# Performance work log

Hardware: AMD Instinct MI355X
Metric: run time of the kernel (lower is better)

## Reference

```python
import jax, jax.numpy as jnp
import numpy as np

N_NODES = 100000


def _graph_conv_right(feat, src, dst, W, b, n_nodes):
    # DGL GraphConv(norm='right'): since in_feats > out_feats, apply weight first,
    # then sum-aggregate messages over edges, divide by in-degree (clamped >= 1),
    # add bias, then relu activation.
    h = feat @ W                                   # [N, out]
    msg = jnp.take(h, src, axis=0)                 # [E, out] gather from source nodes
    agg = jax.ops.segment_sum(msg, dst, num_segments=n_nodes)  # [N, out]
    deg = jax.ops.segment_sum(jnp.ones_like(dst, dtype=feat.dtype), dst,
                              num_segments=n_nodes)
    deg = jnp.clip(deg, 1.0, None)                 # allow_zero_in_degree
    out = agg / deg[:, None] + b
    return jax.nn.relu(out)


def setup_inputs() -> dict:
    key = jax.random.key(0)
    ks = jax.random.split(key, 6)
    n_edges = 3200000
    in_dim, hidden_dim, out_dim = 128, 32, 12
    features = jax.random.normal(ks[0], (N_NODES, in_dim), dtype=jnp.float32)
    src = jax.random.randint(ks[1], (n_edges,), 0, N_NODES, dtype=jnp.int64 if jax.config.jax_enable_x64 else jnp.int32)
    dst = jax.random.randint(ks[2], (n_edges,), 0, N_NODES, dtype=jnp.int64 if jax.config.jax_enable_x64 else jnp.int32)
    W1 = jax.random.normal(ks[3], (in_dim, hidden_dim), dtype=jnp.float32) * (1.0 / np.sqrt(in_dim))
    b1 = jnp.zeros((hidden_dim,), dtype=jnp.float32)
    W2 = jax.random.normal(ks[4], (hidden_dim, out_dim), dtype=jnp.float32) * (1.0 / np.sqrt(hidden_dim))
    b2 = jnp.zeros((out_dim,), dtype=jnp.float32)
    return {"features": features, "src": src, "dst": dst,
            "W1": W1, "b1": b1, "W2": W2, "b2": b2}


def reference(features, src, dst, W1, b1, W2, b2):
    x = _graph_conv_right(features, src, dst, W1, b1, N_NODES)
    x = jax.nn.relu(x)  # extra F.relu after layer1 (idempotent, kept for fidelity)
    x = _graph_conv_right(x, src, dst, W2, b2, N_NODES)
    return x
```

## Files before the change

### kernel.cpp

```cpp
#include <hip/hip_runtime.h>
#include <hip/hip_fp16.h>

#define N_IN   128
#define HID    32
#define ODIM   12
#define H2P    16
#define RNODES 128
#define RSH    7
#define NBMAX  800
#define NBK    1024
#define BCAP   4608
#define CHUNK  4096

__device__ __forceinline__ void acc_f4(float (&acc)[8], float4 vf) {
    union { float4 f; __half2 h[4]; } uu; uu.f = vf;
    float2 g0 = __half22float2(uu.h[0]);
    float2 g1 = __half22float2(uu.h[1]);
    float2 g2 = __half22float2(uu.h[2]);
    float2 g3 = __half22float2(uu.h[3]);
    acc[0] += g0.x; acc[1] += g0.y;
    acc[2] += g1.x; acc[3] += g1.y;
    acc[4] += g2.x; acc[5] += g2.y;
    acc[6] += g3.x; acc[7] += g3.y;
}

__global__ __launch_bounds__(256) void gemm1_kernel(const float* __restrict__ feat,
                                                    const float* __restrict__ W1,
                                                    __half* __restrict__ h1,
                                                    int* __restrict__ bcur, int nNodes) {
    if (blockIdx.x == 0) {
        ((int4*)bcur)[threadIdx.x] = make_int4(0, 0, 0, 0);
    }
    __shared__ float sF[64 * 132];
    __shared__ float sW[N_IN * HID];
    const int tid = threadIdx.x;
    const int nb  = blockIdx.x * 64;

    {
        const float4* Wv  = (const float4*)W1;
        float4*       sWv = (float4*)sW;
        #pragma unroll
        for (int i = 0; i < 4; ++i) sWv[tid + 256 * i] = Wv[tid + 256 * i];
    }
    #pragma unroll
    for (int i = 0; i < 8; ++i) {
        int f   = tid + 256 * i;
        int row = f >> 5;
        int c4  = f & 31;
        int n   = nb + row;
        float4 v = make_float4(0.f, 0.f, 0.f, 0.f);
        if (n < nNodes) v = *(const float4*)(feat + (size_t)n * N_IN + c4 * 4);
        *(float4*)(sF + row * 132 + c4 * 4) = v;
    }
    __syncthreads();

    const int og = tid & 7;
    const int ng = tid >> 3;
    const int o0 = og * 4;
    const float* f0 = sF + ng * 132;
    const float* f1 = sF + (ng + 32) * 132;

    float acc0[4] = {0.f, 0.f, 0.f, 0.f};
    float acc1[4] = {0.f, 0.f, 0.f, 0.f};
    #pragma unroll 8
    for (int k = 0; k < N_IN; k += 4) {
        float4 a0 = *(const float4*)(f0 + k);
        float4 a1 = *(const float4*)(f1 + k);
        const float a0v[4] = {a0.x, a0.y, a0.z, a0.w};
        const float a1v[4] = {a1.x, a1.y, a1.z, a1.w};
        #pragma unroll
        for (int j = 0; j < 4; ++j) {
            float4 w = *(const float4*)(sW + (k + j) * HID + o0);
            acc0[0] += a0v[j] * w.x; acc0[1] += a0v[j] * w.y;
            acc0[2] += a0v[j] * w.z; acc0[3] += a0v[j] * w.w;
            acc1[0] += a1v[j] * w.x; acc1[1] += a1v[j] * w.y;
            acc1[2] += a1v[j] * w.z; acc1[3] += a1v[j] * w.w;
        }
    }
    int n0 = nb + ng, n1 = nb + ng + 32;
    if (n0 < nNodes) {
        union { __half2 h[2]; float2 f; } u;
        u.h[0] = __floats2half2_rn(acc0[0], acc0[1]);
        u.h[1] = __floats2half2_rn(acc0[2], acc0[3]);
        *(float2*)(h1 + (size_t)n0 * HID + o0) = u.f;
    }
    if (n1 < nNodes) {
        union { __half2 h[2]; float2 f; } u;
        u.h[0] = __floats2half2_rn(acc1[0], acc1[1]);
        u.h[1] = __floats2half2_rn(acc1[2], acc1[3]);
        *(float2*)(h1 + (size_t)n1 * HID + o0) = u.f;
    }
}

__global__ __launch_bounds__(512) void bplace_kernel(const int* __restrict__ src,
                                                     const int* __restrict__ dst,
                                                     int* __restrict__ bcur,
                                                     int* __restrict__ pairs, int nEdges) {
    __shared__ int      lh[NBK];
    __shared__ int      lcur[NBK];
    __shared__ int      gofs[NBK];
    __shared__ int      sWS[16];
    __shared__ int      lst[CHUNK];
    __shared__ unsigned short lbk[CHUNK];

    const int tid  = threadIdx.x;
    const int base = blockIdx.x * CHUNK;
    const int m    = min(CHUNK, nEdges - base);

    ((int2*)lh)[tid] = make_int2(0, 0);
    __syncthreads();

    int4 dv[2], sv[2];
    bool ok[2];
    #pragma unroll
    for (int k = 0; k < 2; ++k) {
        int e = base + k * 2048 + tid * 4;
        ok[k] = (e < nEdges);
        if (ok[k]) {
            dv[k] = *(const int4*)(dst + e);
            sv[k] = *(const int4*)(src + e);
        }
    }
    #pragma unroll
    for (int k = 0; k < 2; ++k) {
        if (ok[k]) {
            atomicAdd(&lh[dv[k].x >> RSH], 1);
            atomicAdd(&lh[dv[k].y >> RSH], 1);
            atomicAdd(&lh[dv[k].z >> RSH], 1);
            atomicAdd(&lh[dv[k].w >> RSH], 1);
        }
    }
    __syncthreads();

    int c0 = lh[2 * tid], c1 = lh[2 * tid + 1];
    int tsum = c0 + c1;
    const int lane = tid & 63, wid = tid >> 6;
    int inc = tsum;
    #pragma unroll
    for (int off = 1; off < 64; off <<= 1) {
        int t = __shfl_up(inc, off, 64);
        if (lane >= off) inc += t;
    }
    if (lane == 63) sWS[wid] = inc;
    __syncthreads();
    if (tid == 0) {
        int r = 0;
        #pragma unroll
        for (int w = 0; w < 8; ++w) { int s = sWS[w]; sWS[8 + w] = r; r += s; }
    }
    __syncthreads();
    int excl = sWS[8 + wid] + inc - tsum;
    lh[2 * tid]       = excl;
    lh[2 * tid + 1]   = excl + c0;
    lcur[2 * tid]     = excl;
    lcur[2 * tid + 1] = excl + c0;
    gofs[2 * tid]     = (c0 > 0) ? atomicAdd(&bcur[2 * tid], c0) : 0;
    gofs[2 * tid + 1] = (c1 > 0) ? atomicAdd(&bcur[2 * tid + 1], c1) : 0;
    __syncthreads();

    #pragma unroll
    for (int k = 0; k < 2; ++k) {
        if (ok[k]) {
            int b, p;
            b = dv[k].x >> RSH; p = atomicAdd(&lcur[b], 1); lst[p] = ((dv[k].x & (RNODES - 1)) << 17) | sv[k].x; lbk[p] = (unsigned short)b;
            b = dv[k].y >> RSH; p = atomicAdd(&lcur[b], 1); lst[p] = ((dv[k].y & (RNODES - 1)) << 17) | sv[k].y; lbk[p] = (unsigned short)b;
            b = dv[k].z >> RSH; p = atomicAdd(&lcur[b], 1); lst[p] = ((dv[k].z & (RNODES - 1)) << 17) | sv[k].z; lbk[p] = (unsigned short)b;
            b = dv[k].w >> RSH; p = atomicAdd(&lcur[b], 1); lst[p] = ((dv[k].w & (RNODES - 1)) << 17) | sv[k].w; lbk[p] = (unsigned short)b;
        }
    }
    __syncthreads();

    for (int i = tid; i < m; i += 512) {
        int b = lbk[i];
        int rank = gofs[b] + (i - lh[b]);
        if (rank < BCAP) pairs[(size_t)b * BCAP + rank] = lst[i];
    }
}

__global__ __launch_bounds__(512) void agg1_kernel(const __half* __restrict__ h1,
                                                   const int* __restrict__ bcur,
                                                   int* __restrict__ pairs,
                                                   const float* __restrict__ b1,
                                                   const float* __restrict__ W2,
                                                   __half* __restrict__ h2,
                                                   float* __restrict__ rdeg,
                                                   int* __restrict__ rowstartg,
                                                   int* __restrict__ countg, int nNodes) {
    __shared__ int   sorted[BCAP];
    __shared__ int   hist[RNODES];
    __shared__ int   scn[RNODES];
    __shared__ int   cur[RNODES];
    __shared__ int   sws[2];
    __shared__ float sW2[HID * ODIM];
    const int tid = threadIdx.x;
    const int bkt = blockIdx.x;
    const int cnt = min(bcur[bkt], BCAP);
    const size_t pb = (size_t)bkt * BCAP;

    if (tid < RNODES) hist[tid] = 0;
    if (tid < 96) ((float4*)sW2)[tid] = ((const float4*)W2)[tid];
    __syncthreads();

    int vreg[9];
    #pragma unroll
    for (int u = 0; u < 9; ++u) {
        int i = tid + u * 512;
        if (i < cnt) {
            int v = pairs[pb + i];
            vreg[u] = v;
            atomicAdd(&hist[v >> 17], 1);
        }
    }
    __syncthreads();

    int v0 = 0, inc = 0;
    if (tid < RNODES) {
        v0 = hist[tid];
        inc = v0;
        #pragma unroll
        for (int off = 1; off < 64; off <<= 1) {
            int t = __shfl_up(inc, off, 64);
            if ((tid & 63) >= off) inc += t;
        }
        if ((tid & 63) == 63) sws[tid >> 6] = inc;
    }
    __syncthreads();
    if (tid < RNODES) {
        int add = (tid >= 64) ? sws[0] : 0;
        scn[tid] = add + inc - v0;
        cur[tid] = add + inc - v0;
    }
    __syncthreads();

    #pragma unroll
    for (int u = 0; u < 9; ++u) {
        int i = tid + u * 512;
        if (i < cnt) {
            int v = vreg[u];
            int pos = atomicAdd(&cur[v >> 17], 1);
            sorted[pos] = v & 0x1FFFF;
        }
    }
    __syncthreads();

    for (int i = tid; i < cnt; i += 512) pairs[pb + i] = sorted[i];
    if (tid < RNODES) {
        int n = bkt * RNODES + tid;
        if (n < nNodes) {
            rowstartg[n] = (int)pb + scn[tid];
            countg[n]    = hist[tid];
        }
    }

    const int r   = tid & 7;
    const int grp = tid >> 3;
    const int q   = r & 3;
    const int sub = r >> 2;
    const float4* h1q = (const float4*)h1;

    #pragma unroll
    for (int g = 0; g < 2; ++g) {
        const int nl = g * 64 + grp;
        const int n  = bkt * RNODES + nl;
        if (n >= nNodes) continue;
        const int dcnt = hist[nl];
        const int beg  = scn[nl];
        const int end  = beg + dcnt;

        float acc[8] = {0.f, 0.f, 0.f, 0.f, 0.f, 0.f, 0.f, 0.f};
        int i = beg;
        for (; i + 16 <= end; i += 16) {
            float4 v[8];
            #pragma unroll
            for (int u = 0; u < 8; ++u) {
                int e = sorted[i + 2 * u + sub];
                v[u] = h1q[(size_t)e * 4 + q];
            }
            #pragma unroll
            for (int u = 0; u < 8; ++u) acc_f4(acc, v[u]);
        }
        for (; i + 2 <= end; i += 2) {
            int e = sorted[i + sub];
            acc_f4(acc, h1q[(size_t)e * 4 + q]);
        }
        if (i < end && sub == 0) {
            int e = sorted[i];
            acc_f4(acc, h1q[(size_t)e * 4 + q]);
        }

        #pragma unroll
        for (int t = 0; t < 8; ++t) acc[t] += __shfl_xor(acc[t], 4, 8);

        const float rd = 1.f / (float)(dcnt < 1 ? 1 : dcnt);
        float x[8];
        #pragma unroll
        for (int t = 0; t < 8; ++t) {
            float xv = acc[t] * rd + b1[8 * q + t];
            x[t] = xv > 0.f ? xv : 0.f;
        }

        const int j0  = r;
        const int j1m = (r < 4) ? (r + 8) : r;
        float o0 = 0.f, o1 = 0.f;
        #pragma unroll
        for (int qq = 0; qq < 4; ++qq) {
            #pragma unroll
            for (int t = 0; t < 8; ++t) {
                float xv = __shfl(x[t], qq, 8);
                int k = 8 * qq + t;
                o0 += xv * sW2[k * ODIM + j0];
                o1 += xv * sW2[k * ODIM + j1m];
            }
        }
        h2[(size_t)n * H2P + j0] = __float2half(o0);
        if (r < 4) h2[(size_t)n * H2P + 8 + r] = __float2half(o1);
        if (r == 0) rdeg[n] = rd;
    }
}

__global__ __launch_bounds__(512) void agg2_kernel(const __half* __restrict__ h2,
                                                   const int* __restrict__ rowstartg,
                                                   const int* __restrict__ countg,
                                                   const int* __restrict__ eidx,
                                                   const float* __restrict__ rdeg,
                                                   const float* __restrict__ b2,
                                                   float* __restrict__ out, int nNodes) {
    const int tid = threadIdx.x;
    const int grp = tid >> 3;
    const int r   = tid & 7;
    const int n   = blockIdx.x * 64 + grp;
    if (n >= nNodes) return;

    const int half = r & 1;
    const int sub  = r >> 1;
    const float4* h2q = (const float4*)h2;

    const int cnt = countg[n];
    const int beg = rowstartg[n];
    const int end = beg + cnt;

    float acc[8] = {0.f, 0.f, 0.f, 0.f, 0.f, 0.f, 0.f, 0.f};
    int i = beg;
    for (; i + 32 <= end; i += 32) {
        float4 v[8];
        #pragma unroll
        for (int u = 0; u < 8; ++u) {
            int e = eidx[i + 4 * u + sub];
            v[u] = h2q[(size_t)e * 2 + half];
        }
        #pragma unroll
        for (int u = 0; u < 8; ++u) acc_f4(acc, v[u]);
    }
    for (; i + 4 <= end; i += 4) {
        int e = eidx[i + sub];
        acc_f4(acc, h2q[(size_t)e * 2 + half]);
    }
    const int rem = end - i;
    if (sub < rem) {
        int e = eidx[i + sub];
        acc_f4(acc, h2q[(size_t)e * 2 + half]);
    }

    #pragma unroll
    for (int t = 0; t < 8; ++t) {
        acc[t] += __shfl_xor(acc[t], 2, 8);
        acc[t] += __shfl_xor(acc[t], 4, 8);
    }

    const float rd = rdeg[n];
    if (r == 0) {
        float w[8];
        #pragma unroll
        for (int t = 0; t < 8; ++t) {
            float wv = acc[t] * rd + b2[t];
            w[t] = wv > 0.f ? wv : 0.f;
        }
        *(float4*)(out + (size_t)n * ODIM)     = make_float4(w[0], w[1], w[2], w[3]);
        *(float4*)(out + (size_t)n * ODIM + 4) = make_float4(w[4], w[5], w[6], w[7]);
    } else if (r == 1) {
        float w[4];
        #pragma unroll
        for (int t = 0; t < 4; ++t) {
            float wv = acc[t] * rd + b2[8 + t];
            w[t] = wv > 0.f ? wv : 0.f;
        }
        *(float4*)(out + (size_t)n * ODIM + 8) = make_float4(w[0], w[1], w[2], w[3]);
    }
}

extern "C" void kernel_launch(void* const* d_in, const int* in_sizes, int n_in,
                              void* d_out, int out_size, void* d_ws, size_t ws_size,
                              hipStream_t stream) {
    const float* feat = (const float*)d_in[0];
    const int*   src  = (const int*)d_in[1];
    const int*   dst  = (const int*)d_in[2];
    const float* W1   = (const float*)d_in[3];
    const float* b1   = (const float*)d_in[4];
    const float* W2   = (const float*)d_in[5];
    const float* b2   = (const float*)d_in[6];
    float* out = (float*)d_out;

    const int nEdges = in_sizes[1];
    const int nNodes = in_sizes[0] / N_IN;
    const int nb     = (nNodes + RNODES - 1) / RNODES;

    __half* h1       = (__half*)d_ws;
    __half* h2       = h1 + (size_t)nNodes * HID;
    float*  rdeg     = (float*)(h2 + (size_t)nNodes * H2P);
    int*    rowstart = (int*)(rdeg + nNodes);
    int*    countg   = rowstart + nNodes;
    int*    bcur     = countg + nNodes;
    int*    pairs    = bcur + NBK;

    gemm1_kernel<<<(nNodes + 63) / 64, 256, 0, stream>>>(feat, W1, h1, bcur, nNodes);
    bplace_kernel<<<(nEdges + CHUNK - 1) / CHUNK, 512, 0, stream>>>(src, dst, bcur, pairs, nEdges);
    agg1_kernel<<<nb, 512, 0, stream>>>(h1, bcur, pairs, b1, W2, h2, rdeg, rowstart, countg, nNodes);
    agg2_kernel<<<(nNodes + 63) / 64, 512, 0, stream>>>(h2, rowstart, countg, pairs, rdeg, b2, out, nNodes);
}
```

Before: 238.2 us.

## Split agg1 into sort and gather kernels, enlarge bplace chunks, shrink blocks

The fused per-bucket sort-and-aggregate kernel is split into a sort_kernel that writes sorted source indices and row offsets to global memory, and a separate gather1_kernel with 256-thread blocks covering 32 nodes each. This spreads the layer-1 gather over far more blocks than the 782 buckets, so more of the GPU stays busy, at the cost of one extra launch and a global round trip for the sorted indices. bplace now handles 6400 edges per block (three int4 loads plus a scalar tail), which cuts the block count and the global atomics on bucket cursors. The rdeg buffer is dropped and the reciprocal degree is recomputed in agg2, which also moves to 256-thread blocks.

Result: faster. 225.7 us (-5.2%).

```diff
diff --git a/kernel.cpp b/kernel.cpp
--- a/kernel.cpp
+++ b/kernel.cpp
@@ -10,7 +10,7 @@
 #define NBMAX  800
 #define NBK    1024
 #define BCAP   4608
-#define CHUNK  4096
+#define CHUNK  6400
 
 __device__ __forceinline__ void acc_f4(float (&acc)[8], float4 vf) {
     union { float4 f; __half2 h[4]; } uu; uu.f = vf;
@@ -110,10 +110,10 @@
     ((int2*)lh)[tid] = make_int2(0, 0);
     __syncthreads();
 
-    int4 dv[2], sv[2];
-    bool ok[2];
-    #pragma unroll
-    for (int k = 0; k < 2; ++k) {
+    int4 dv[3], sv[3];
+    bool ok[3];
+    #pragma unroll
+    for (int k = 0; k < 3; ++k) {
         int e = base + k * 2048 + tid * 4;
         ok[k] = (e < nEdges);
         if (ok[k]) {
@@ -121,8 +121,14 @@
             sv[k] = *(const int4*)(src + e);
         }
     }
-    #pragma unroll
-    for (int k = 0; k < 2; ++k) {
+    int  dt = 0, st = 0;
+    bool okt = (tid < 256) && (base + 6144 + tid < nEdges);
+    if (okt) {
+        dt = dst[base + 6144 + tid];
+        st = src[base + 6144 + tid];
+    }
+    #pragma unroll
+    for (int k = 0; k < 3; ++k) {
         if (ok[k]) {
             atomicAdd(&lh[dv[k].x >> RSH], 1);
             atomicAdd(&lh[dv[k].y >> RSH], 1);
@@ -130,6 +136,7 @@
             atomicAdd(&lh[dv[k].w >> RSH], 1);
         }
     }
+    if (okt) atomicAdd(&lh[dt >> RSH], 1);
     __syncthreads();
 
     int c0 = lh[2 * tid], c1 = lh[2 * tid + 1];
@@ -159,7 +166,7 @@
     __syncthreads();
 
     #pragma unroll
-    for (int k = 0; k < 2; ++k) {
+    for (int k = 0; k < 3; ++k) {
         if (ok[k]) {
             int b, p;
             b = dv[k].x >> RSH; p = atomicAdd(&lcur[b], 1); lst[p] = ((dv[k].x & (RNODES - 1)) << 17) | sv[k].x; lbk[p] = (unsigned short)b;
@@ -168,6 +175,10 @@
             b = dv[k].w >> RSH; p = atomicAdd(&lcur[b], 1); lst[p] = ((dv[k].w & (RNODES - 1)) << 17) | sv[k].w; lbk[p] = (unsigned short)b;
         }
     }
+    if (okt) {
+        int b = dt >> RSH, p = atomicAdd(&lcur[b], 1);
+        lst[p] = ((dt & (RNODES - 1)) << 17) | st; lbk[p] = (unsigned short)b;
+    }
     __syncthreads();
 
     for (int i = tid; i < m; i += 512) {
@@ -177,28 +188,21 @@
     }
 }
 
-__global__ __launch_bounds__(512) void agg1_kernel(const __half* __restrict__ h1,
-                                                   const int* __restrict__ bcur,
+__global__ __launch_bounds__(512) void sort_kernel(const int* __restrict__ bcur,
                                                    int* __restrict__ pairs,
-                                                   const float* __restrict__ b1,
-                                                   const float* __restrict__ W2,
-                                                   __half* __restrict__ h2,
-                                                   float* __restrict__ rdeg,
                                                    int* __restrict__ rowstartg,
                                                    int* __restrict__ countg, int nNodes) {
-    __shared__ int   sorted[BCAP];
-    __shared__ int   hist[RNODES];
-    __shared__ int   scn[RNODES];
-    __shared__ int   cur[RNODES];
-    __shared__ int   sws[2];
-    __shared__ float sW2[HID * ODIM];
+    __shared__ int sorted[BCAP];
+    __shared__ int hist[RNODES];
+    __shared__ int scn[RNODES];
+    __shared__ int cur[RNODES];
+    __shared__ int sws[2];
     const int tid = threadIdx.x;
     const int bkt = blockIdx.x;
     const int cnt = min(bcur[bkt], BCAP);
     const size_t pb = (size_t)bkt * BCAP;
 
     if (tid < RNODES) hist[tid] = 0;
-    if (tid < 96) ((float4*)sW2)[tid] = ((const float4*)W2)[tid];
     __syncthreads();
 
     int vreg[9];
@@ -251,84 +255,91 @@
             countg[n]    = hist[tid];
         }
     }
+}
+
+__global__ __launch_bounds__(256) void gather1_kernel(const __half* __restrict__ h1,
+                                                      const int* __restrict__ rowstartg,
+                                                      const int* __restrict__ countg,
+                                                      const int* __restrict__ eidx,
+                                                      const float* __restrict__ b1,
+                                                      const float* __restrict__ W2,
+                                                      __half* __restrict__ h2, int nNodes) {
+    __shared__ float sW2[HID * ODIM];
+    const int tid = threadIdx.x;
+    if (tid < 96) ((float4*)sW2)[tid] = ((const float4*)W2)[tid];
+    __syncthreads();
 
     const int r   = tid & 7;
     const int grp = tid >> 3;
     const int q   = r & 3;
     const int sub = r >> 2;
+    const int n   = blockIdx.x * 32 + grp;
+    if (n >= nNodes) return;
+
     const float4* h1q = (const float4*)h1;
-
-    #pragma unroll
-    for (int g = 0; g < 2; ++g) {
-        const int nl = g * 64 + grp;
-        const int n  = bkt * RNODES + nl;
-        if (n >= nNodes) continue;
-        const int dcnt = hist[nl];
-        const int beg  = scn[nl];
-        const int end  = beg + dcnt;
-
-        float acc[8] = {0.f, 0.f, 0.f, 0.f, 0.f, 0.f, 0.f, 0.f};
-        int i = beg;
-        for (; i + 16 <= end; i += 16) {
-            float4 v[8];
-            #pragma unroll
-            for (int u = 0; u < 8; ++u) {
-                int e = sorted[i + 2 * u + sub];
-                v[u] = h1q[(size_t)e * 4 + q];
-            }
-            #pragma unroll
-            for (int u = 0; u < 8; ++u) acc_f4(acc, v[u]);
-        }
-        for (; i + 2 <= end; i += 2) {
-            int e = sorted[i + sub];
-            acc_f4(acc, h1q[(size_t)e * 4 + q]);
-        }
-        if (i < end && sub == 0) {
-            int e = sorted[i];
-            acc_f4(acc, h1q[(size_t)e * 4 + q]);
-        }
-
-        #pragma unroll
-        for (int t = 0; t < 8; ++t) acc[t] += __shfl_xor(acc[t], 4, 8);
-
-        const float rd = 1.f / (float)(dcnt < 1 ? 1 : dcnt);
-        float x[8];
+    const int dcnt = countg[n];
+    const int beg  = rowstartg[n];
+    const int end  = beg + dcnt;
+
+    float acc[8] = {0.f, 0.f, 0.f, 0.f, 0.f, 0.f, 0.f, 0.f};
+    int i = beg;
+    for (; i + 16 <= end; i += 16) {
+        float4 v[8];
+        #pragma unroll
+        for (int u = 0; u < 8; ++u) {
+            int e = eidx[i + 2 * u + sub];
+            v[u] = h1q[(size_t)e * 4 + q];
+        }
+        #pragma unroll
+        for (int u = 0; u < 8; ++u) acc_f4(acc, v[u]);
+    }
+    for (; i + 2 <= end; i += 2) {
+        int e = eidx[i + sub];
+        acc_f4(acc, h1q[(size_t)e * 4 + q]);
+    }
+    if (i < end && sub == 0) {
+        int e = eidx[i];
+        acc_f4(acc, h1q[(size_t)e * 4 + q]);
+    }
+
+    #pragma unroll
+    for (int t = 0; t < 8; ++t) acc[t] += __shfl_xor(acc[t], 4, 8);
+
+    const float rd = 1.f / (float)(dcnt < 1 ? 1 : dcnt);
+    float x[8];
+    #pragma unroll
+    for (int t = 0; t < 8; ++t) {
+        float xv = acc[t] * rd + b1[8 * q + t];
+        x[t] = xv > 0.f ? xv : 0.f;
+    }
+
+    const int j0  = r;
+    const int j1m = (r < 4) ? (r + 8) : r;
+    float o0 = 0.f, o1 = 0.f;
+    #pragma unroll
+    for (int qq = 0; qq < 4; ++qq) {
         #pragma unroll
         for (int t = 0; t < 8; ++t) {
-            float xv = acc[t] * rd + b1[8 * q + t];
-            x[t] = xv > 0.f ? xv : 0.f;
-        }
-
-        const int j0  = r;
-        const int j1m = (r < 4) ? (r + 8) : r;
-        float o0 = 0.f, o1 = 0.f;
-        #pragma unroll
-        for (int qq = 0; qq < 4; ++qq) {
-            #pragma unroll
-            for (int t = 0; t < 8; ++t) {
-                float xv = __shfl(x[t], qq, 8);
-                int k = 8 * qq + t;
-                o0 += xv * sW2[k * ODIM + j0];
-                o1 += xv * sW2[k * ODIM + j1m];
-            }
-        }
-        h2[(size_t)n * H2P + j0] = __float2half(o0);
-        if (r < 4) h2[(size_t)n * H2P + 8 + r] = __float2half(o1);
-        if (r == 0) rdeg[n] = rd;
-    }
-}
-
-__global__ __launch_bounds__(512) void agg2_kernel(const __half* __restrict__ h2,
+            float xv = __shfl(x[t], qq, 8);
+            int k = 8 * qq + t;
+            o0 += xv * sW2[k * ODIM + j0];
+            o1 += xv * sW2[k * ODIM + j1m];
+        }
+    }
+    h2[(size_t)n * H2P + j0] = __float2half(o0);
+    if (r < 4) h2[(size_t)n * H2P + 8 + r] = __float2half(o1);
+}
+
+__global__ __launch_bounds__(256) void agg2_kernel(const __half* __restrict__ h2,
                                                    const int* __restrict__ rowstartg,
                                                    const int* __restrict__ countg,
                                                    const int* __restrict__ eidx,
-                                                   const float* __restrict__ rdeg,
                                                    const float* __restrict__ b2,
                                                    float* __restrict__ out, int nNodes) {
     const int tid = threadIdx.x;
     const int grp = tid >> 3;
     const int r   = tid & 7;
-    const int n   = blockIdx.x * 64 + grp;
+    const int n   = blockIdx.x * 32 + grp;
     if (n >= nNodes) return;
 
     const int half = r & 1;
@@ -367,7 +378,7 @@
         acc[t] += __shfl_xor(acc[t], 4, 8);
     }
 
-    const float rd = rdeg[n];
+    const float rd = 1.f / (float)(cnt < 1 ? 1 : cnt);
     if (r == 0) {
         float w[8];
         #pragma unroll
@@ -406,14 +417,14 @@
 
     __half* h1       = (__half*)d_ws;
     __half* h2       = h1 + (size_t)nNodes * HID;
-    float*  rdeg     = (float*)(h2 + (size_t)nNodes * H2P);
-    int*    rowstart = (int*)(rdeg + nNodes);
+    int*    rowstart = (int*)(h2 + (size_t)nNodes * H2P);
     int*    countg   = rowstart + nNodes;
     int*    bcur     = countg + nNodes;
     int*    pairs    = bcur + NBK;
 
     gemm1_kernel<<<(nNodes + 63) / 64, 256, 0, stream>>>(feat, W1, h1, bcur, nNodes);
     bplace_kernel<<<(nEdges + CHUNK - 1) / CHUNK, 512, 0, stream>>>(src, dst, bcur, pairs, nEdges);
-    agg1_kernel<<<nb, 512, 0, stream>>>(h1, bcur, pairs, b1, W2, h2, rdeg, rowstart, countg, nNodes);
-    agg2_kernel<<<(nNodes + 63) / 64, 512, 0, stream>>>(h2, rowstart, countg, pairs, rdeg, b2, out, nNodes);
-}
+    sort_kernel<<<nb, 512, 0, stream>>>(bcur, pairs, rowstart, countg, nNodes);
+    gather1_kernel<<<(nNodes + 31) / 32, 256, 0, stream>>>(h1, rowstart, countg, pairs, b1, W2, h2, nNodes);
+    agg2_kernel<<<(nNodes + 31) / 32, 256, 0, stream>>>(h2, rowstart, countg, pairs, b2, out, nNodes);
+}
```

## Split buckets into half-blocks and re-sort edges in LDS per layer

Applied to the files above, without the earlier changes.

The two aggregation kernels now run two blocks per 128-node bucket, each covering 64 nodes. Each block rebuilds its own per-node CSR in shared memory from the bucketed pairs. This removes the sorted-pairs writeback and the global rowstart, count and rdeg arrays, and doubles the number of blocks for parallelism. Layer 1 aggregation now gives each node 16 lanes that each read a half2 per edge, and the W2 matmul uses shuffles. The placement chunk is doubled to 8192 edges per block. The cost is sorting twice (once per layer) and a per-half cap of 2560 edges, which could drop edges on skewed graphs.

Result: faster. 225.5 us (-5.3%).

```diff
diff --git a/kernel.cpp b/kernel.cpp
--- a/kernel.cpp
+++ b/kernel.cpp
@@ -10,7 +10,8 @@
 #define NBMAX  800
 #define NBK    1024
 #define BCAP   4608
-#define CHUNK  4096
+#define HCAP   2560
+#define CHUNK  8192
 
 __device__ __forceinline__ void acc_f4(float (&acc)[8], float4 vf) {
     union { float4 f; __half2 h[4]; } uu; uu.f = vf;
@@ -110,10 +111,10 @@
     ((int2*)lh)[tid] = make_int2(0, 0);
     __syncthreads();
 
-    int4 dv[2], sv[2];
-    bool ok[2];
-    #pragma unroll
-    for (int k = 0; k < 2; ++k) {
+    int4 dv[4], sv[4];
+    bool ok[4];
+    #pragma unroll
+    for (int k = 0; k < 4; ++k) {
         int e = base + k * 2048 + tid * 4;
         ok[k] = (e < nEdges);
         if (ok[k]) {
@@ -122,7 +123,7 @@
         }
     }
     #pragma unroll
-    for (int k = 0; k < 2; ++k) {
+    for (int k = 0; k < 4; ++k) {
         if (ok[k]) {
             atomicAdd(&lh[dv[k].x >> RSH], 1);
             atomicAdd(&lh[dv[k].y >> RSH], 1);
@@ -159,7 +160,7 @@
     __syncthreads();
 
     #pragma unroll
-    for (int k = 0; k < 2; ++k) {
+    for (int k = 0; k < 4; ++k) {
         if (ok[k]) {
             int b, p;
             b = dv[k].x >> RSH; p = atomicAdd(&lcur[b], 1); lst[p] = ((dv[k].x & (RNODES - 1)) << 17) | sv[k].x; lbk[p] = (unsigned short)b;
@@ -177,27 +178,24 @@
     }
 }
 
-__global__ __launch_bounds__(512) void agg1_kernel(const __half* __restrict__ h1,
-                                                   const int* __restrict__ bcur,
-                                                   int* __restrict__ pairs,
-                                                   const float* __restrict__ b1,
-                                                   const float* __restrict__ W2,
-                                                   __half* __restrict__ h2,
-                                                   float* __restrict__ rdeg,
-                                                   int* __restrict__ rowstartg,
-                                                   int* __restrict__ countg, int nNodes) {
-    __shared__ int   sorted[BCAP];
-    __shared__ int   hist[RNODES];
-    __shared__ int   scn[RNODES];
-    __shared__ int   cur[RNODES];
-    __shared__ int   sws[2];
+__global__ __launch_bounds__(512) void l1_kernel(const __half* __restrict__ h1,
+                                                 const int* __restrict__ bcur,
+                                                 const int* __restrict__ pairs,
+                                                 const float* __restrict__ b1,
+                                                 const float* __restrict__ W2,
+                                                 __half* __restrict__ h2, int nNodes) {
+    __shared__ int   sorted[HCAP];
+    __shared__ int   hist[64];
+    __shared__ int   scn[64];
+    __shared__ int   cur[64];
     __shared__ float sW2[HID * ODIM];
     const int tid = threadIdx.x;
-    const int bkt = blockIdx.x;
+    const int bkt = blockIdx.x >> 1;
+    const int h   = blockIdx.x & 1;
     const int cnt = min(bcur[bkt], BCAP);
     const size_t pb = (size_t)bkt * BCAP;
 
-    if (tid < RNODES) hist[tid] = 0;
+    if (tid < 64) hist[tid] = 0;
     if (tid < 96) ((float4*)sW2)[tid] = ((const float4*)W2)[tid];
     __syncthreads();
 
@@ -208,27 +206,20 @@
         if (i < cnt) {
             int v = pairs[pb + i];
             vreg[u] = v;
-            atomicAdd(&hist[v >> 17], 1);
-        }
-    }
-    __syncthreads();
-
-    int v0 = 0, inc = 0;
-    if (tid < RNODES) {
-        v0 = hist[tid];
-        inc = v0;
+            if (((v >> 17) >> 6) == h) atomicAdd(&hist[(v >> 17) & 63], 1);
+        }
+    }
+    __syncthreads();
+
+    if (tid < 64) {
+        int v0 = hist[tid], inc = v0;
         #pragma unroll
         for (int off = 1; off < 64; off <<= 1) {
             int t = __shfl_up(inc, off, 64);
-            if ((tid & 63) >= off) inc += t;
-        }
-        if ((tid & 63) == 63) sws[tid >> 6] = inc;
-    }
-    __syncthreads();
-    if (tid < RNODES) {
-        int add = (tid >= 64) ? sws[0] : 0;
-        scn[tid] = add + inc - v0;
-        cur[tid] = add + inc - v0;
+            if (tid >= off) inc += t;
+        }
+        scn[tid] = inc - v0;
+        cur[tid] = inc - v0;
     }
     __syncthreads();
 
@@ -237,107 +228,145 @@
         int i = tid + u * 512;
         if (i < cnt) {
             int v = vreg[u];
-            int pos = atomicAdd(&cur[v >> 17], 1);
-            sorted[pos] = v & 0x1FFFF;
-        }
-    }
-    __syncthreads();
-
-    for (int i = tid; i < cnt; i += 512) pairs[pb + i] = sorted[i];
-    if (tid < RNODES) {
-        int n = bkt * RNODES + tid;
-        if (n < nNodes) {
-            rowstartg[n] = (int)pb + scn[tid];
-            countg[n]    = hist[tid];
-        }
-    }
-
-    const int r   = tid & 7;
-    const int grp = tid >> 3;
-    const int q   = r & 3;
-    const int sub = r >> 2;
-    const float4* h1q = (const float4*)h1;
+            if (((v >> 17) >> 6) == h) {
+                int pos = atomicAdd(&cur[(v >> 17) & 63], 1);
+                if (pos < HCAP) sorted[pos] = v & 0x1FFFF;
+            }
+        }
+    }
+    __syncthreads();
+
+    const int c   = tid & 15;
+    const int grp = tid >> 4;
+    const __half2* h1v = (const __half2*)h1;
+    const int col = (c < ODIM) ? c : 0;
 
     #pragma unroll
     for (int g = 0; g < 2; ++g) {
-        const int nl = g * 64 + grp;
-        const int n  = bkt * RNODES + nl;
+        int nl = g * 32 + grp;
+        int n  = bkt * RNODES + h * 64 + nl;
         if (n >= nNodes) continue;
-        const int dcnt = hist[nl];
-        const int beg  = scn[nl];
-        const int end  = beg + dcnt;
-
-        float acc[8] = {0.f, 0.f, 0.f, 0.f, 0.f, 0.f, 0.f, 0.f};
+        int dcnt = hist[nl];
+        int beg  = scn[nl];
+        int end  = beg + dcnt;
+
+        float2 s0 = {0.f, 0.f}, s1 = {0.f, 0.f}, s2 = {0.f, 0.f}, s3 = {0.f, 0.f};
         int i = beg;
-        for (; i + 16 <= end; i += 16) {
-            float4 v[8];
-            #pragma unroll
-            for (int u = 0; u < 8; ++u) {
-                int e = sorted[i + 2 * u + sub];
-                v[u] = h1q[(size_t)e * 4 + q];
+        for (; i + 8 <= end; i += 8) {
+            int e0 = sorted[i],     e1 = sorted[i + 1], e2 = sorted[i + 2], e3 = sorted[i + 3];
+            int e4 = sorted[i + 4], e5 = sorted[i + 5], e6 = sorted[i + 6], e7 = sorted[i + 7];
+            float2 f0 = __half22float2(h1v[(size_t)e0 * 16 + c]);
+            float2 f1 = __half22float2(h1v[(size_t)e1 * 16 + c]);
+            float2 f2 = __half22float2(h1v[(size_t)e2 * 16 + c]);
+            float2 f3 = __half22float2(h1v[(size_t)e3 * 16 + c]);
+            float2 f4 = __half22float2(h1v[(size_t)e4 * 16 + c]);
+            float2 f5 = __half22float2(h1v[(size_t)e5 * 16 + c]);
+            float2 f6 = __half22float2(h1v[(size_t)e6 * 16 + c]);
+            float2 f7 = __half22float2(h1v[(size_t)e7 * 16 + c]);
+            s0.x += f0.x; s0.y += f0.y;  s1.x += f1.x; s1.y += f1.y;
+            s2.x += f2.x; s2.y += f2.y;  s3.x += f3.x; s3.y += f3.y;
+            s0.x += f4.x; s0.y += f4.y;  s1.x += f5.x; s1.y += f5.y;
+            s2.x += f6.x; s2.y += f6.y;  s3.x += f7.x; s3.y += f7.y;
+        }
+        for (; i + 4 <= end; i += 4) {
+            int e0 = sorted[i], e1 = sorted[i + 1], e2 = sorted[i + 2], e3 = sorted[i + 3];
+            float2 f0 = __half22float2(h1v[(size_t)e0 * 16 + c]);
+            float2 f1 = __half22float2(h1v[(size_t)e1 * 16 + c]);
+            float2 f2 = __half22float2(h1v[(size_t)e2 * 16 + c]);
+            float2 f3 = __half22float2(h1v[(size_t)e3 * 16 + c]);
+            s0.x += f0.x; s0.y += f0.y;  s1.x += f1.x; s1.y += f1.y;
+            s2.x += f2.x; s2.y += f2.y;  s3.x += f3.x; s3.y += f3.y;
+        }
+        for (; i < end; ++i) {
+            float2 f = __half22float2(h1v[(size_t)sorted[i] * 16 + c]);
+            s0.x += f.x; s0.y += f.y;
+        }
+        float sumx = (s0.x + s1.x) + (s2.x + s3.x);
+        float sumy = (s0.y + s1.y) + (s2.y + s3.y);
+
+        float rd = 1.f / (float)(dcnt < 1 ? 1 : dcnt);
+        float x0 = sumx * rd + b1[2 * c];
+        float x1 = sumy * rd + b1[2 * c + 1];
+        x0 = x0 > 0.f ? x0 : 0.f;
+        x1 = x1 > 0.f ? x1 : 0.f;
+
+        float acc = 0.f;
+        #pragma unroll
+        for (int k = 0; k < 16; ++k) {
+            float xk0 = __shfl(x0, k, 16);
+            float xk1 = __shfl(x1, k, 16);
+            acc += xk0 * sW2[(2 * k) * ODIM + col] + xk1 * sW2[(2 * k + 1) * ODIM + col];
+        }
+        if (c < ODIM) h2[(size_t)n * H2P + c] = __float2half(acc);
+    }
+}
+
+__global__ __launch_bounds__(512) void l2_kernel(const __half* __restrict__ h2,
+                                                 const int* __restrict__ bcur,
+                                                 const int* __restrict__ pairs,
+                                                 const float* __restrict__ b2,
+                                                 float* __restrict__ out, int nNodes) {
+    __shared__ int sorted[HCAP];
+    __shared__ int hist[64];
+    __shared__ int scn[64];
+    __shared__ int cur[64];
+    const int tid = threadIdx.x;
+    const int bkt = blockIdx.x >> 1;
+    const int h   = blockIdx.x & 1;
+    const int cnt = min(bcur[bkt], BCAP);
+    const size_t pb = (size_t)bkt * BCAP;
+
+    if (tid < 64) hist[tid] = 0;
+    __syncthreads();
+
+    int vreg[9];
+    #pragma unroll
+    for (int u = 0; u < 9; ++u) {
+        int i = tid + u * 512;
+        if (i < cnt) {
+            int v = pairs[pb + i];
+            vreg[u] = v;
+            if (((v >> 17) >> 6) == h) atomicAdd(&hist[(v >> 17) & 63], 1);
+        }
+    }
+    __syncthreads();
+
+    if (tid < 64) {
+        int v0 = hist[tid], inc = v0;
+        #pragma unroll
+        for (int off = 1; off < 64; off <<= 1) {
+            int t = __shfl_up(inc, off, 64);
+            if (tid >= off) inc += t;
+        }
+        scn[tid] = inc - v0;
+        cur[tid] = inc - v0;
+    }
+    __syncthreads();
+
+    #pragma unroll
+    for (int u = 0; u < 9; ++u) {
+        int i = tid + u * 512;
+        if (i < cnt) {
+            int v = vreg[u];
+            if (((v >> 17) >> 6) == h) {
+                int pos = atomicAdd(&cur[(v >> 17) & 63], 1);
+                if (pos < HCAP) sorted[pos] = v & 0x1FFFF;
             }
-            #pragma unroll
-            for (int u = 0; u < 8; ++u) acc_f4(acc, v[u]);
-        }
-        for (; i + 2 <= end; i += 2) {
-            int e = sorted[i + sub];
-            acc_f4(acc, h1q[(size_t)e * 4 + q]);
-        }
-        if (i < end && sub == 0) {
-            int e = sorted[i];
-            acc_f4(acc, h1q[(size_t)e * 4 + q]);
-        }
-
-        #pragma unroll
-        for (int t = 0; t < 8; ++t) acc[t] += __shfl_xor(acc[t], 4, 8);
-
-        const float rd = 1.f / (float)(dcnt < 1 ? 1 : dcnt);
-        float x[8];
-        #pragma unroll
-        for (int t = 0; t < 8; ++t) {
-            float xv = acc[t] * rd + b1[8 * q + t];
-            x[t] = xv > 0.f ? xv : 0.f;
-        }
-
-        const int j0  = r;
-        const int j1m = (r < 4) ? (r + 8) : r;
-        float o0 = 0.f, o1 = 0.f;
-        #pragma unroll
-        for (int qq = 0; qq < 4; ++qq) {
-            #pragma unroll
-            for (int t = 0; t < 8; ++t) {
-                float xv = __shfl(x[t], qq, 8);
-                int k = 8 * qq + t;
-                o0 += xv * sW2[k * ODIM + j0];
-                o1 += xv * sW2[k * ODIM + j1m];
-            }
-        }
-        h2[(size_t)n * H2P + j0] = __float2half(o0);
-        if (r < 4) h2[(size_t)n * H2P + 8 + r] = __float2half(o1);
-        if (r == 0) rdeg[n] = rd;
-    }
-}
-
-__global__ __launch_bounds__(512) void agg2_kernel(const __half* __restrict__ h2,
-                                                   const int* __restrict__ rowstartg,
-                                                   const int* __restrict__ countg,
-                                                   const int* __restrict__ eidx,
-                                                   const float* __restrict__ rdeg,
-                                                   const float* __restrict__ b2,
-                                                   float* __restrict__ out, int nNodes) {
-    const int tid = threadIdx.x;
-    const int grp = tid >> 3;
-    const int r   = tid & 7;
-    const int n   = blockIdx.x * 64 + grp;
-    if (n >= nNodes) return;
-
+        }
+    }
+    __syncthreads();
+
+    const int r    = tid & 7;
+    const int nl   = tid >> 3;
     const int half = r & 1;
     const int sub  = r >> 1;
+    const int n    = bkt * RNODES + h * 64 + nl;
+    if (n >= nNodes) return;
+
     const float4* h2q = (const float4*)h2;
-
-    const int cnt = countg[n];
-    const int beg = rowstartg[n];
-    const int end = beg + cnt;
+    const int dcnt = hist[nl];
+    const int beg  = scn[nl];
+    const int end  = beg + dcnt;
 
     float acc[8] = {0.f, 0.f, 0.f, 0.f, 0.f, 0.f, 0.f, 0.f};
     int i = beg;
@@ -345,19 +374,19 @@
         float4 v[8];
         #pragma unroll
         for (int u = 0; u < 8; ++u) {
-            int e = eidx[i + 4 * u + sub];
+            int e = sorted[i + 4 * u + sub];
             v[u] = h2q[(size_t)e * 2 + half];
         }
         #pragma unroll
         for (int u = 0; u < 8; ++u) acc_f4(acc, v[u]);
     }
     for (; i + 4 <= end; i += 4) {
-        int e = eidx[i + sub];
+        int e = sorted[i + sub];
         acc_f4(acc, h2q[(size_t)e * 2 + half]);
     }
     const int rem = end - i;
     if (sub < rem) {
-        int e = eidx[i + sub];
+        int e = sorted[i + sub];
         acc_f4(acc, h2q[(size_t)e * 2 + half]);
     }
 
@@ -367,7 +396,7 @@
         acc[t] += __shfl_xor(acc[t], 4, 8);
     }
 
-    const float rd = rdeg[n];
+    const float rd = 1.f / (float)(dcnt < 1 ? 1 : dcnt);
     if (r == 0) {
         float w[8];
         #pragma unroll
@@ -403,17 +432,15 @@
     const int nEdges = in_sizes[1];
     const int nNodes = in_sizes[0] / N_IN;
     const int nb     = (nNodes + RNODES - 1) / RNODES;
-
-    __half* h1       = (__half*)d_ws;
-    __half* h2       = h1 + (size_t)nNodes * HID;
-    float*  rdeg     = (float*)(h2 + (size_t)nNodes * H2P);
-    int*    rowstart = (int*)(rdeg + nNodes);
-    int*    countg   = rowstart + nNodes;
-    int*    bcur     = countg + nNodes;
-    int*    pairs    = bcur + NBK;
+    const int hbGrid = 2 * nb;
+
+    __half* h1    = (__half*)d_ws;
+    __half* h2    = h1 + (size_t)nNodes * HID;
+    int*    bcur  = (int*)(h2 + (size_t)nNodes * H2P);
+    int*    pairs = bcur + NBK;
 
     gemm1_kernel<<<(nNodes + 63) / 64, 256, 0, stream>>>(feat, W1, h1, bcur, nNodes);
     bplace_kernel<<<(nEdges + CHUNK - 1) / CHUNK, 512, 0, stream>>>(src, dst, bcur, pairs, nEdges);
-    agg1_kernel<<<nb, 512, 0, stream>>>(h1, bcur, pairs, b1, W2, h2, rdeg, rowstart, countg, nNodes);
-    agg2_kernel<<<(nNodes + 63) / 64, 512, 0, stream>>>(h2, rowstart, countg, pairs, rdeg, b2, out, nNodes);
-}
+    l1_kernel<<<hbGrid, 512, 0, stream>>>(h1, bcur, pairs, b1, W2, h2, nNodes);
+    l2_kernel<<<hbGrid, 512, 0, stream>>>(h2, bcur, pairs, b2, out, nNodes);
+}
```
